# Performance work log

Hardware: AMD Instinct MI355X
Metric: run time of the kernel (lower is better)

## Reference

```python
import jax, jax.numpy as jnp
import numpy as np

N = 50000
E = 800000
IN_DIM = 128
HEADS = 4
OUT_DIM = 32
TOT = HEADS * OUT_DIM  # 128 == IN_DIM -> residual_proj is None
LN_EPS = 1e-5
NEG_SLOPE = 0.2


def setup_inputs() -> dict:
    key = jax.random.key(0)
    ks = jax.random.split(key, 10)
    x = jax.random.normal(ks[0], (N, IN_DIM), dtype=jnp.float32)
    # random edges guaranteed src != dst (PyG GATv2Conv removes then re-adds self loops)
    src = jax.random.randint(ks[1], (E,), 0, N)
    off = jax.random.randint(ks[2], (E,), 1, N)
    dst = (src + off) % N
    edge_index = jnp.stack([src, dst]).astype(jnp.int64)
    # glorot-style init for weights
    sc = 1.0 / np.sqrt(IN_DIM)
    W_l = jax.random.uniform(ks[3], (IN_DIM, TOT), jnp.float32, -sc, sc)
    b_l = jnp.zeros((TOT,), jnp.float32)
    W_r = jax.random.uniform(ks[4], (IN_DIM, TOT), jnp.float32, -sc, sc)
    b_r = jnp.zeros((TOT,), jnp.float32)
    att = jax.random.uniform(ks[5], (HEADS, OUT_DIM), jnp.float32, -sc, sc)
    bias = jnp.zeros((TOT,), jnp.float32)
    ln_g = jnp.ones((TOT,), jnp.float32)
    ln_b = jnp.zeros((TOT,), jnp.float32)
    return {"x": x, "edge_index": edge_index, "W_l": W_l, "b_l": b_l,
            "W_r": W_r, "b_r": b_r, "att": att, "bias": bias,
            "ln_g": ln_g, "ln_b": ln_b}


def _gatv2_layer(x, src, dst, W_l, b_l, W_r, b_r, att, bias, ln_g, ln_b):
    n = x.shape[0]
    # GATv2Conv: x_l = lin_l(x) (source/messages), x_r = lin_r(x) (target)
    xl = (x @ W_l + b_l).reshape(n, HEADS, OUT_DIM)
    xr = (x @ W_r + b_r).reshape(n, HEADS, OUT_DIM)
    m = xl[src] + xr[dst]                               # [E+N, H, D]
    s = jnp.einsum('ehd,hd->eh', jax.nn.leaky_relu(m, NEG_SLOPE), att)
    # per-destination softmax (every node has a self loop -> no empty segments)
    smax = jax.ops.segment_max(s, dst, num_segments=n)  # [N, H]
    e = jnp.exp(s - smax[dst])
    denom = jax.ops.segment_sum(e, dst, num_segments=n)
    alpha = e / denom[dst]                              # [E+N, H]
    out = jax.ops.segment_sum(alpha[..., None] * xl[src], dst, num_segments=n)
    out = out.reshape(n, TOT) + bias
    out = out + x                                       # residual (in_dim == total_out_dim)
    mu = jnp.mean(out, axis=-1, keepdims=True)
    var = jnp.mean(jnp.square(out - mu), axis=-1, keepdims=True)
    y = (out - mu) / jnp.sqrt(var + LN_EPS) * ln_g + ln_b
    return jax.nn.elu(y)


def reference(x, edge_index, W_l, b_l, W_r, b_r, att, bias, ln_g, ln_b):
    n = x.shape[0]
    loops = jnp.arange(n, dtype=edge_index.dtype)
    src = jnp.concatenate([edge_index[0], loops])
    dst = jnp.concatenate([edge_index[1], loops])
    return _gatv2_layer(x, src, dst, W_l, b_l, W_r, b_r, att, bias, ln_g, ln_b)
```

## Files before the change

### kernel.cpp

```cpp
#include <hip/hip_runtime.h>

#define N_NODES 50000
#define E_EDGES 800000
#define M_TOTAL (E_EDGES + N_NODES)
#define IN_DIM 128
#define HEADS 4
#define OUT_DIM 32
#define TOT 128
#define LN_EPS 1e-5f
#define NEG_SLOPE 0.2f
#define LOG2E 1.4426950408889634f

#define SCAN_NBLK ((N_NODES + 255) / 256)
#define GEMM_NBLK ((N_NODES + 63) / 64)
#define HIST_NBLK 128
#define EPB 6656

typedef __bf16 bf16x8 __attribute__((ext_vector_type(8)));
typedef float  f32x4  __attribute__((ext_vector_type(4)));
typedef _Float16 h2   __attribute__((ext_vector_type(2)));

__device__ __forceinline__ float quad_sum(float p) {
    p += __int_as_float(__builtin_amdgcn_update_dpp(
        0, __float_as_int(p), 0xB1 , 0xF, 0xF, true));
    p += __int_as_float(__builtin_amdgcn_update_dpp(
        0, __float_as_int(p), 0x4E , 0xF, 0xF, true));
    return p;
}

__global__ __launch_bounds__(256) void wthist_kernel(
    const int* __restrict__ dsts,
    const float* __restrict__ Wl, const float* __restrict__ Wr,
    unsigned* __restrict__ WT, unsigned char* __restrict__ HP,
    unsigned char* __restrict__ rank8) {
    __shared__ unsigned cnt[N_NODES / 4];
    const int b = blockIdx.x, t = threadIdx.x;
    if (b < 64) {
        const int u = b * 256 + t;
        const int col = u >> 6, k2 = u & 63;
        const float* __restrict__ W = (col < 128) ? Wl : Wr;
        const int c = col & 127;
        union { __bf16 bb[2]; unsigned uu; } p;
        p.bb[0] = (__bf16)W[(2 * k2) * TOT + c];
        p.bb[1] = (__bf16)W[(2 * k2 + 1) * TOT + c];
        WT[col * 64 + k2] = p.uu;
        return;
    }
    const int hb = b - 64;
    const int m_begin = hb * EPB;
    const int m_end = min(m_begin + EPB, M_TOTAL);
    for (int i = t; i < N_NODES / 4; i += 256) cnt[i] = 0;
    __syncthreads();
    for (int m0 = m_begin + t * 4; m0 < m_end; m0 += 1024) {
        int d[4];
        if (m0 < E_EDGES) {
            const int4 dv = *(const int4*)&dsts[m0];
            d[0] = dv.x; d[1] = dv.y; d[2] = dv.z; d[3] = dv.w;
        } else {
            d[0] = m0 - E_EDGES; d[1] = d[0] + 1; d[2] = d[0] + 2; d[3] = d[0] + 3;
        }
        uchar4 r;
        unsigned old, sh;
        sh = (d[0] & 3) * 8; old = atomicAdd(&cnt[d[0] >> 2], 1u << sh);
        r.x = (unsigned char)(old >> sh);
        sh = (d[1] & 3) * 8; old = atomicAdd(&cnt[d[1] >> 2], 1u << sh);
        r.y = (unsigned char)(old >> sh);
        sh = (d[2] & 3) * 8; old = atomicAdd(&cnt[d[2] >> 2], 1u << sh);
        r.z = (unsigned char)(old >> sh);
        sh = (d[3] & 3) * 8; old = atomicAdd(&cnt[d[3] >> 2], 1u << sh);
        r.w = (unsigned char)(old >> sh);
        *(uchar4*)&rank8[m0] = r;
    }
    __syncthreads();
    unsigned* __restrict__ Hrow = (unsigned*)(HP + (size_t)hb * N_NODES);
    for (int i = t; i < N_NODES / 4; i += 256) Hrow[i] = cnt[i];
}

__global__ __launch_bounds__(256) void gemm_kernel(
    const float* __restrict__ x, const unsigned* __restrict__ WT,
    const float* __restrict__ bl, const float* __restrict__ br,
    unsigned* __restrict__ xlb, unsigned* __restrict__ xrb) {
    __shared__ float epi[4][16][66];
    __shared__ unsigned Bs[64][68];
    const int t = threadIdx.x, w = t >> 6, lane = t & 63;
    const int q = lane >> 4, ln = lane & 15;
    const int m0 = blockIdx.x * 64;

    const int row = min(m0 + w * 16 + ln, N_NODES - 1);
    const float* __restrict__ xrow = x + (size_t)row * IN_DIM;
    bf16x8 A[4];
#pragma unroll
    for (int c = 0; c < 4; ++c) {
        const float4 v0 = *(const float4*)&xrow[c * 32 + q * 8];
        const float4 v1 = *(const float4*)&xrow[c * 32 + q * 8 + 4];
        bf16x8 a;
        a[0] = (__bf16)v0.x; a[1] = (__bf16)v0.y; a[2] = (__bf16)v0.z; a[3] = (__bf16)v0.w;
        a[4] = (__bf16)v1.x; a[5] = (__bf16)v1.y; a[6] = (__bf16)v1.z; a[7] = (__bf16)v1.w;
        A[c] = a;
    }

    const int mr = lane >> 2, cg2 = (lane & 3) * 16;
    const int grow = m0 + w * 16 + mr;
#pragma unroll
    for (int g = 0; g < 4; ++g) {
        const int n0 = g * 64;
        __syncthreads();
        {
            const unsigned* __restrict__ src = WT + n0 * 64;
#pragma unroll
            for (int it = 0; it < 4; ++it) {
                const int dw = t * 4 + it * 1024;
                const uint4 v = *(const uint4*)&src[dw];
                *(uint4*)&Bs[dw >> 6][dw & 63] = v;
            }
        }
        __syncthreads();
        const float* __restrict__ bvec = (g < 2) ? bl : br;
        f32x4 acc[4];
#pragma unroll
        for (int nt = 0; nt < 4; ++nt) {
            const float b = bvec[(n0 & 127) + nt * 16 + ln];
            acc[nt] = (f32x4){b, b, b, b};
        }
#pragma unroll
        for (int nt = 0; nt < 4; ++nt) {
#pragma unroll
            for (int c = 0; c < 4; ++c) {
                const bf16x8 B = *(const bf16x8*)&Bs[nt * 16 + ln][c * 16 + q * 4];
                acc[nt] = __builtin_amdgcn_mfma_f32_16x16x32_bf16(A[c], B, acc[nt], 0, 0, 0);
            }
        }
#pragma unroll
        for (int nt = 0; nt < 4; ++nt)
#pragma unroll
            for (int r = 0; r < 4; ++r)
                epi[w][q * 4 + r][nt * 16 + ln] = acc[nt][r];

        if (grow < N_NODES) {
            unsigned p[8];
#pragma unroll
            for (int i = 0; i < 8; ++i) {
                union { _Float16 h[2]; unsigned u; } pk;
                pk.h[0] = (_Float16)epi[w][mr][cg2 + 2 * i];
                pk.h[1] = (_Float16)epi[w][mr][cg2 + 2 * i + 1];
                p[i] = pk.u;
            }
            unsigned* __restrict__ dst = ((g < 2) ? xlb : xrb) +
                (size_t)grow * 64 + (g & 1) * 32 + (cg2 >> 1);
            *(uint4*)&dst[0] = make_uint4(p[0], p[1], p[2], p[3]);
            *(uint4*)&dst[4] = make_uint4(p[4], p[5], p[6], p[7]);
        }
    }
}

__global__ __launch_bounds__(256) void scan1_kernel(
    unsigned char* __restrict__ HP,
    int* __restrict__ incl, int* __restrict__ blockSums,
    int* __restrict__ degtot) {
    __shared__ int sh[256];
    const int t = threadIdx.x;
    const int i = blockIdx.x * 256 + t;
    int tot = 0;
    if (i < N_NODES) {
        int run = 0;
#pragma unroll 16
        for (int b = 0; b < HIST_NBLK; ++b) {
            const int h = HP[(size_t)b * N_NODES + i];
            HP[(size_t)b * N_NODES + i] = (unsigned char)run;
            run += h;
        }
        tot = run;
        degtot[i] = tot;
    }
    sh[t] = tot;
    __syncthreads();
#pragma unroll
    for (int off = 1; off < 256; off <<= 1) {
        int u = (t >= off) ? sh[t - off] : 0;
        __syncthreads();
        sh[t] += u;
        __syncthreads();
    }
    if (i < N_NODES) incl[i] = sh[t];
    if (t == 255) blockSums[blockIdx.x] = sh[255];
}

__global__ __launch_bounds__(256) void scan23_kernel(
    const int* __restrict__ degtot, const int* __restrict__ blockSums,
    int* __restrict__ rowptr ,
    unsigned short* __restrict__ sorted16) {
    __shared__ int sh[256];
    const int t = threadIdx.x;
    const int v0 = (t < SCAN_NBLK) ? blockSums[t] : 0;
    sh[t] = v0;
    __syncthreads();
#pragma unroll
    for (int off = 1; off < 256; off <<= 1) {
        int u = (t >= off) ? sh[t - off] : 0;
        __syncthreads();
        sh[t] += u;
        __syncthreads();
    }
    const int blockOff = (blockIdx.x == 0) ? 0 : sh[blockIdx.x - 1];
    const int i = blockIdx.x * 256 + t;
    if (i < N_NODES)
        rowptr[i] = blockOff + rowptr[i] - degtot[i];
    if (i == 0) rowptr[N_NODES] = M_TOTAL;
    if (blockIdx.x == 0 && t < 32) sorted16[M_TOTAL + t] = 0;
}

__global__ __launch_bounds__(1024) void scatter_kernel(
    const int* __restrict__ srcs, const int* __restrict__ dsts,
    const int* __restrict__ rowptr, const unsigned char* __restrict__ P,
    const unsigned char* __restrict__ rank8,
    unsigned short* __restrict__ sorted16) {
    __shared__ __align__(16) unsigned char smem[N_NODES];
    const int t = threadIdx.x;
    const int hb = blockIdx.x;
    const uint4* __restrict__ Prow = (const uint4*)(P + (size_t)hb * N_NODES);
    for (int i = t; i < N_NODES / 16; i += 1024)
        ((uint4*)smem)[i] = Prow[i];
    __syncthreads();
    const int eb = hb * EPB;
    const int ee = min(eb + EPB, M_TOTAL);
    for (int m0 = eb + t * 4; m0 < ee; m0 += 4096) {
        int s[4], d[4];
        if (m0 < E_EDGES) {
            const int4 sv = *(const int4*)&srcs[m0];
            const int4 dv = *(const int4*)&dsts[m0];
            s[0] = sv.x; s[1] = sv.y; s[2] = sv.z; s[3] = sv.w;
            d[0] = dv.x; d[1] = dv.y; d[2] = dv.z; d[3] = dv.w;
        } else {
            s[0] = d[0] = m0 - E_EDGES;
            s[1] = d[1] = d[0] + 1; s[2] = d[2] = d[0] + 2; s[3] = d[3] = d[0] + 3;
        }
        const uchar4 r = *(const uchar4*)&rank8[m0];
        sorted16[rowptr[d[0]] + (int)smem[d[0]] + (int)r.x] = (unsigned short)s[0];
        sorted16[rowptr[d[1]] + (int)smem[d[1]] + (int)r.y] = (unsigned short)s[1];
        sorted16[rowptr[d[2]] + (int)smem[d[2]] + (int)r.z] = (unsigned short)s[2];
        sorted16[rowptr[d[3]] + (int)smem[d[3]] + (int)r.w] = (unsigned short)s[3];
    }
}

__global__ __launch_bounds__(256) void gat_kernel(
    const int* __restrict__ rowptr, const unsigned short* __restrict__ sorted16,
    const unsigned* __restrict__ xlb, const unsigned* __restrict__ xrb,
    const float* __restrict__ att, const float* __restrict__ x,
    const float* __restrict__ bias, const float* __restrict__ g,
    const float* __restrict__ bvec, float* __restrict__ out) {
    const int d = blockIdx.x * 4 + (threadIdx.x >> 6);
    const int lane = threadIdx.x & 63;
    const int ln = lane & 15, q = lane >> 4;
    if (d >= N_NODES) return;

    h2 xrh[4], ath[4];
    {
        const uint4 ur = *(const uint4*)&xrb[(size_t)d * 64 + 4 * ln];
        union { uint4 u; h2 h[4]; } cr; cr.u = ur;
        xrh[0] = cr.h[0]; xrh[1] = cr.h[1]; xrh[2] = cr.h[2]; xrh[3] = cr.h[3];
        const float4 a0 = *(const float4*)&att[8 * ln];
        const float4 a1 = *(const float4*)&att[8 * ln + 4];
        ath[0][0] = (_Float16)(a0.x * LOG2E); ath[0][1] = (_Float16)(a0.y * LOG2E);
        ath[1][0] = (_Float16)(a0.z * LOG2E); ath[1][1] = (_Float16)(a0.w * LOG2E);
        ath[2][0] = (_Float16)(a1.x * LOG2E); ath[2][1] = (_Float16)(a1.y * LOG2E);
        ath[3][0] = (_Float16)(a1.z * LOG2E); ath[3][1] = (_Float16)(a1.w * LOG2E);
    }
    const h2 slope = (h2){(_Float16)NEG_SLOPE, (_Float16)NEG_SLOPE};
    const int beg = rowptr[d], end = rowptr[d + 1];

    float l = 0.f;
    h2 acc4[4];
#pragma unroll
    for (int k = 0; k < 4; ++k) acc4[k] = (h2){(_Float16)0.f, (_Float16)0.f};

    uint4 u0, u1;
    {
        const int sA0 = (int)sorted16[min(beg + q, end - 1)];
        const int sA1 = (int)sorted16[min(beg + 4 + q, end - 1)];
        u0 = *(const uint4*)&xlb[(size_t)sA0 * 64 + 4 * ln];
        u1 = *(const uint4*)&xlb[(size_t)sA1 * 64 + 4 * ln];
    }
    int sB0 = (int)sorted16[min(beg + 8 + q, end - 1)];
    int sB1 = (int)sorted16[min(beg + 12 + q, end - 1)];

    for (int base = beg; base < end; base += 8) {
        const int sC0 = (int)sorted16[min(base + 16 + q, end - 1)];
        const int sC1 = (int)sorted16[min(base + 20 + q, end - 1)];
        const uint4 un0 = *(const uint4*)&xlb[(size_t)sB0 * 64 + 4 * ln];
        const uint4 un1 = *(const uint4*)&xlb[(size_t)sB1 * 64 + 4 * ln];

        union { unsigned uu; h2 h; } a0, a1, a2, a3, b0, b1, b2, b3;
        a0.uu = u0.x; a1.uu = u0.y; a2.uu = u0.z; a3.uu = u0.w;
        b0.uu = u1.x; b1.uu = u1.y; b2.uu = u1.z; b3.uu = u1.w;
        h2 mA0 = a0.h + xrh[0], mA1 = a1.h + xrh[1];
        h2 mA2 = a2.h + xrh[2], mA3 = a3.h + xrh[3];
        h2 mB0 = b0.h + xrh[0], mB1 = b1.h + xrh[1];
        h2 mB2 = b2.h + xrh[2], mB3 = b3.h + xrh[3];
        mA0 = __builtin_elementwise_max(mA0, mA0 * slope);
        mA1 = __builtin_elementwise_max(mA1, mA1 * slope);
        mA2 = __builtin_elementwise_max(mA2, mA2 * slope);
        mA3 = __builtin_elementwise_max(mA3, mA3 * slope);
        mB0 = __builtin_elementwise_max(mB0, mB0 * slope);
        mB1 = __builtin_elementwise_max(mB1, mB1 * slope);
        mB2 = __builtin_elementwise_max(mB2, mB2 * slope);
        mB3 = __builtin_elementwise_max(mB3, mB3 * slope);
        float p0 = __builtin_amdgcn_fdot2(mA0, ath[0], 0.0f, false);
        p0 = __builtin_amdgcn_fdot2(mA1, ath[1], p0, false);
        p0 = __builtin_amdgcn_fdot2(mA2, ath[2], p0, false);
        p0 = __builtin_amdgcn_fdot2(mA3, ath[3], p0, false);
        float p1 = __builtin_amdgcn_fdot2(mB0, ath[0], 0.0f, false);
        p1 = __builtin_amdgcn_fdot2(mB1, ath[1], p1, false);
        p1 = __builtin_amdgcn_fdot2(mB2, ath[2], p1, false);
        p1 = __builtin_amdgcn_fdot2(mB3, ath[3], p1, false);
        p0 = quad_sum(p0);
        p1 = quad_sum(p1);
        const float e0 = (base + q < end) ? exp2f(p0) : 0.f;
        const float e1 = (base + 4 + q < end) ? exp2f(p1) : 0.f;
        l += e0 + e1;
        const _Float16 eh0 = (_Float16)e0, eh1 = (_Float16)e1;
        const h2 e20 = (h2){eh0, eh0}, e21 = (h2){eh1, eh1};
        acc4[0] += e20 * a0.h; acc4[0] += e21 * b0.h;
        acc4[1] += e20 * a1.h; acc4[1] += e21 * b1.h;
        acc4[2] += e20 * a2.h; acc4[2] += e21 * b2.h;
        acc4[3] += e20 * a3.h; acc4[3] += e21 * b3.h;

        u0 = un0; u1 = un1; sB0 = sC0; sB1 = sC1;
    }

#pragma unroll
    for (int off = 16; off <= 32; off <<= 1) {
        l += __shfl_xor(l, off, 64);
#pragma unroll
        for (int k = 0; k < 4; ++k) {
            union { h2 h; int i; } tmp; tmp.h = acc4[k];
            tmp.i = __shfl_xor(tmp.i, off, 64);
            acc4[k] += tmp.h;
        }
    }
    float acc[8];
#pragma unroll
    for (int k = 0; k < 4; ++k) {
        acc[2 * k]     = (float)acc4[k][0];
        acc[2 * k + 1] = (float)acc4[k][1];
    }

    const float inv_l = 1.0f / l;
    const float4 xv0 = *(const float4*)&x[(size_t)d * TOT + 8 * ln];
    const float4 xv1 = *(const float4*)&x[(size_t)d * TOT + 8 * ln + 4];
    const float4 bi0 = *(const float4*)&bias[8 * ln];
    const float4 bi1 = *(const float4*)&bias[8 * ln + 4];
    float v[8];
    v[0] = fmaf(acc[0], inv_l, bi0.x + xv0.x);
    v[1] = fmaf(acc[1], inv_l, bi0.y + xv0.y);
    v[2] = fmaf(acc[2], inv_l, bi0.z + xv0.z);
    v[3] = fmaf(acc[3], inv_l, bi0.w + xv0.w);
    v[4] = fmaf(acc[4], inv_l, bi1.x + xv1.x);
    v[5] = fmaf(acc[5], inv_l, bi1.y + xv1.y);
    v[6] = fmaf(acc[6], inv_l, bi1.z + xv1.z);
    v[7] = fmaf(acc[7], inv_l, bi1.w + xv1.w);
    float sum = 0.f, sq = 0.f;
#pragma unroll
    for (int k = 0; k < 8; ++k) { sum += v[k]; sq = fmaf(v[k], v[k], sq); }
#pragma unroll
    for (int off = 1; off <= 8; off <<= 1) {
        sum += __shfl_xor(sum, off, 64);
        sq  += __shfl_xor(sq,  off, 64);
    }
    const float mu  = sum * (1.0f / TOT);
    const float var = sq * (1.0f / TOT) - mu * mu;
    const float inv = rsqrtf(var + LN_EPS);
    const float4 g0 = *(const float4*)&g[8 * ln];
    const float4 g1 = *(const float4*)&g[8 * ln + 4];
    const float4 b0 = *(const float4*)&bvec[8 * ln];
    const float4 b1 = *(const float4*)&bvec[8 * ln + 4];
    float y[8];
    y[0] = (v[0] - mu) * inv * g0.x + b0.x;
    y[1] = (v[1] - mu) * inv * g0.y + b0.y;
    y[2] = (v[2] - mu) * inv * g0.z + b0.z;
    y[3] = (v[3] - mu) * inv * g0.w + b0.w;
    y[4] = (v[4] - mu) * inv * g1.x + b1.x;
    y[5] = (v[5] - mu) * inv * g1.y + b1.y;
    y[6] = (v[6] - mu) * inv * g1.z + b1.z;
    y[7] = (v[7] - mu) * inv * g1.w + b1.w;
#pragma unroll
    for (int k = 0; k < 8; ++k) y[k] = y[k] > 0.f ? y[k] : __expf(y[k]) - 1.f;
    if (q < 2) {
        float4 o = (q == 0) ? make_float4(y[0], y[1], y[2], y[3])
                            : make_float4(y[4], y[5], y[6], y[7]);
        *(float4*)&out[(size_t)d * TOT + 8 * ln + 4 * q] = o;
    }
}

extern "C" void kernel_launch(void* const* d_in, const int* in_sizes, int n_in,
                              void* d_out, int out_size, void* d_ws, size_t ws_size,
                              hipStream_t stream) {
    const float* x    = (const float*)d_in[0];
    const int*   ei   = (const int*)d_in[1];
    const float* Wl   = (const float*)d_in[2];
    const float* bl   = (const float*)d_in[3];
    const float* Wr   = (const float*)d_in[4];
    const float* br   = (const float*)d_in[5];
    const float* att  = (const float*)d_in[6];
    const float* bias = (const float*)d_in[7];
    const float* ln_g = (const float*)d_in[8];
    const float* ln_b = (const float*)d_in[9];
    const int* srcs = ei;
    const int* dsts = ei + E_EDGES;

    unsigned* xlb = (unsigned*)d_ws;
    unsigned* xrb = xlb + (size_t)N_NODES * 64;
    int*   degtot     = (int*)(xrb + (size_t)N_NODES * 64);
    int*   rowptr     = degtot + N_NODES;
    int*   blockSums  = rowptr + N_NODES + 1;
    unsigned* WT      = (unsigned*)(blockSums + SCAN_NBLK + 3);
    unsigned char* HP = (unsigned char*)(WT + 256 * 64);
    unsigned short* sorted16 = (unsigned short*)(HP + (size_t)HIST_NBLK * N_NODES);
    unsigned char*  rank8    = (unsigned char*)(sorted16 + M_TOTAL + 32);

    wthist_kernel<<<64 + HIST_NBLK, 256, 0, stream>>>(dsts, Wl, Wr, WT, HP, rank8);
    gemm_kernel<<<GEMM_NBLK, 256, 0, stream>>>(x, WT, bl, br, xlb, xrb);
    scan1_kernel<<<SCAN_NBLK, 256, 0, stream>>>(HP, rowptr, blockSums, degtot);
    scan23_kernel<<<SCAN_NBLK, 256, 0, stream>>>(degtot, blockSums, rowptr, sorted16);
    scatter_kernel<<<HIST_NBLK, 1024, 0, stream>>>(srcs, dsts, rowptr, HP, rank8, sorted16);
    gat_kernel<<<(N_NODES + 3) / 4, 256, 0, stream>>>(rowptr, sorted16, xlb, xrb, att, x,
                                                      bias, ln_g, ln_b, (float*)d_out);
}
```

Measured before the change: 175.3 us.

## Fuse histogram and GEMM into one launch with 4-bit shared counters

Merges the weight-transpose/histogram kernel and the GEMM kernel into a single launch. Histogram blocks run alongside GEMM blocks, and each GEMM block converts fp32 weights to bf16 in LDS itself, so the WT workspace goes away. The histogram now packs per-node counts as 4-bit nibbles, halving LDS use so histogram blocks can share occupancy with GEMM blocks. The nibble counts overflow if any node gets 16 or more edges within one block's chunk; with random edges that is unlikely but not guaranteed. The gat kernel also issues its epilogue parameter loads early to hide their latency.

```diff
diff --git a/kernel.cpp b/kernel.cpp
--- a/kernel.cpp
+++ b/kernel.cpp
@@ -28,61 +28,57 @@
     return p;
 }
 
-__global__ __launch_bounds__(256) void wthist_kernel(
+__global__ __launch_bounds__(256) void histgemm_kernel(
     const int* __restrict__ dsts,
     const float* __restrict__ Wl, const float* __restrict__ Wr,
-    unsigned* __restrict__ WT, unsigned char* __restrict__ HP,
-    unsigned char* __restrict__ rank8) {
-    __shared__ unsigned cnt[N_NODES / 4];
-    const int b = blockIdx.x, t = threadIdx.x;
-    if (b < 64) {
-        const int u = b * 256 + t;
-        const int col = u >> 6, k2 = u & 63;
-        const float* __restrict__ W = (col < 128) ? Wl : Wr;
-        const int c = col & 127;
-        union { __bf16 bb[2]; unsigned uu; } p;
-        p.bb[0] = (__bf16)W[(2 * k2) * TOT + c];
-        p.bb[1] = (__bf16)W[(2 * k2 + 1) * TOT + c];
-        WT[col * 64 + k2] = p.uu;
-        return;
-    }
-    const int hb = b - 64;
-    const int m_begin = hb * EPB;
-    const int m_end = min(m_begin + EPB, M_TOTAL);
-    for (int i = t; i < N_NODES / 4; i += 256) cnt[i] = 0;
-    __syncthreads();
-    for (int m0 = m_begin + t * 4; m0 < m_end; m0 += 1024) {
-        int d[4];
-        if (m0 < E_EDGES) {
-            const int4 dv = *(const int4*)&dsts[m0];
-            d[0] = dv.x; d[1] = dv.y; d[2] = dv.z; d[3] = dv.w;
-        } else {
-            d[0] = m0 - E_EDGES; d[1] = d[0] + 1; d[2] = d[0] + 2; d[3] = d[0] + 3;
-        }
-        uchar4 r;
-        unsigned old, sh;
-        sh = (d[0] & 3) * 8; old = atomicAdd(&cnt[d[0] >> 2], 1u << sh);
-        r.x = (unsigned char)(old >> sh);
-        sh = (d[1] & 3) * 8; old = atomicAdd(&cnt[d[1] >> 2], 1u << sh);
-        r.y = (unsigned char)(old >> sh);
-        sh = (d[2] & 3) * 8; old = atomicAdd(&cnt[d[2] >> 2], 1u << sh);
-        r.z = (unsigned char)(old >> sh);
-        sh = (d[3] & 3) * 8; old = atomicAdd(&cnt[d[3] >> 2], 1u << sh);
-        r.w = (unsigned char)(old >> sh);
-        *(uchar4*)&rank8[m0] = r;
-    }
-    __syncthreads();
-    unsigned* __restrict__ Hrow = (unsigned*)(HP + (size_t)hb * N_NODES);
-    for (int i = t; i < N_NODES / 4; i += 256) Hrow[i] = cnt[i];
-}
-
-__global__ __launch_bounds__(256) void gemm_kernel(
-    const float* __restrict__ x, const unsigned* __restrict__ WT,
+    unsigned char* __restrict__ HP, unsigned char* __restrict__ rank8,
+    const float* __restrict__ x,
     const float* __restrict__ bl, const float* __restrict__ br,
     unsigned* __restrict__ xlb, unsigned* __restrict__ xrb) {
-    __shared__ float epi[4][16][66];
-    __shared__ unsigned Bs[64][68];
-    const int t = threadIdx.x, w = t >> 6, lane = t & 63;
+    __shared__ union {
+        unsigned cnt[N_NODES / 8];
+        struct { float epi[4][16][66]; unsigned Bs[64][68]; } g;
+    } sm;
+    const int t = threadIdx.x;
+    if (blockIdx.x >= GEMM_NBLK) {
+        const int hb = blockIdx.x - GEMM_NBLK;
+        const int m_begin = hb * EPB;
+        const int m_end = min(m_begin + EPB, M_TOTAL);
+        for (int i = t; i < N_NODES / 8; i += 256) sm.cnt[i] = 0;
+        __syncthreads();
+        for (int m0 = m_begin + t * 4; m0 < m_end; m0 += 1024) {
+            int d[4];
+            if (m0 < E_EDGES) {
+                const int4 dv = *(const int4*)&dsts[m0];
+                d[0] = dv.x; d[1] = dv.y; d[2] = dv.z; d[3] = dv.w;
+            } else {
+                d[0] = m0 - E_EDGES; d[1] = d[0] + 1; d[2] = d[0] + 2; d[3] = d[0] + 3;
+            }
+            uchar4 r;
+            unsigned old, sh;
+            sh = (d[0] & 7) * 4; old = atomicAdd(&sm.cnt[d[0] >> 3], 1u << sh);
+            r.x = (unsigned char)((old >> sh) & 15u);
+            sh = (d[1] & 7) * 4; old = atomicAdd(&sm.cnt[d[1] >> 3], 1u << sh);
+            r.y = (unsigned char)((old >> sh) & 15u);
+            sh = (d[2] & 7) * 4; old = atomicAdd(&sm.cnt[d[2] >> 3], 1u << sh);
+            r.z = (unsigned char)((old >> sh) & 15u);
+            sh = (d[3] & 7) * 4; old = atomicAdd(&sm.cnt[d[3] >> 3], 1u << sh);
+            r.w = (unsigned char)((old >> sh) & 15u);
+            *(uchar4*)&rank8[m0] = r;
+        }
+        __syncthreads();
+        unsigned* __restrict__ Hrow = (unsigned*)(HP + (size_t)hb * N_NODES);
+        for (int i = t; i < N_NODES / 8; i += 256) {
+            const unsigned w = sm.cnt[i];
+            const unsigned lo = (w & 15u) | (((w >> 4) & 15u) << 8) |
+                                (((w >> 8) & 15u) << 16) | (((w >> 12) & 15u) << 24);
+            const unsigned hi = ((w >> 16) & 15u) | (((w >> 20) & 15u) << 8) |
+                                (((w >> 24) & 15u) << 16) | (((w >> 28) & 15u) << 24);
+            *(uint2*)&Hrow[2 * i] = make_uint2(lo, hi);
+        }
+        return;
+    }
+    const int w = t >> 6, lane = t & 63;
     const int q = lane >> 4, ln = lane & 15;
     const int m0 = blockIdx.x * 64;
 
@@ -103,30 +99,34 @@
     const int grow = m0 + w * 16 + mr;
 #pragma unroll
     for (int g = 0; g < 4; ++g) {
-        const int n0 = g * 64;
-        __syncthreads();
-        {
-            const unsigned* __restrict__ src = WT + n0 * 64;
-#pragma unroll
-            for (int it = 0; it < 4; ++it) {
-                const int dw = t * 4 + it * 1024;
-                const uint4 v = *(const uint4*)&src[dw];
-                *(uint4*)&Bs[dw >> 6][dw & 63] = v;
-            }
+        const float* __restrict__ Wsrc = (g < 2) ? Wl : Wr;
+        const int cbase = (g & 1) * 64;
+        __syncthreads();
+#pragma unroll
+        for (int it = 0; it < 4; ++it) {
+            const int cell = t + it * 256;
+            const int k2 = cell >> 4, c = (cell & 15) * 4;
+            const float4 a = *(const float4*)&Wsrc[(2 * k2) * TOT + cbase + c];
+            const float4 b = *(const float4*)&Wsrc[(2 * k2 + 1) * TOT + cbase + c];
+            union { __bf16 bb[2]; unsigned uu; } p;
+            p.bb[0] = (__bf16)a.x; p.bb[1] = (__bf16)b.x; sm.g.Bs[c][k2] = p.uu;
+            p.bb[0] = (__bf16)a.y; p.bb[1] = (__bf16)b.y; sm.g.Bs[c + 1][k2] = p.uu;
+            p.bb[0] = (__bf16)a.z; p.bb[1] = (__bf16)b.z; sm.g.Bs[c + 2][k2] = p.uu;
+            p.bb[0] = (__bf16)a.w; p.bb[1] = (__bf16)b.w; sm.g.Bs[c + 3][k2] = p.uu;
         }
         __syncthreads();
         const float* __restrict__ bvec = (g < 2) ? bl : br;
         f32x4 acc[4];
 #pragma unroll
         for (int nt = 0; nt < 4; ++nt) {
-            const float b = bvec[(n0 & 127) + nt * 16 + ln];
+            const float b = bvec[cbase + nt * 16 + ln];
             acc[nt] = (f32x4){b, b, b, b};
         }
 #pragma unroll
         for (int nt = 0; nt < 4; ++nt) {
 #pragma unroll
             for (int c = 0; c < 4; ++c) {
-                const bf16x8 B = *(const bf16x8*)&Bs[nt * 16 + ln][c * 16 + q * 4];
+                const bf16x8 B = *(const bf16x8*)&sm.g.Bs[nt * 16 + ln][c * 16 + q * 4];
                 acc[nt] = __builtin_amdgcn_mfma_f32_16x16x32_bf16(A[c], B, acc[nt], 0, 0, 0);
             }
         }
@@ -134,15 +134,15 @@
         for (int nt = 0; nt < 4; ++nt)
 #pragma unroll
             for (int r = 0; r < 4; ++r)
-                epi[w][q * 4 + r][nt * 16 + ln] = acc[nt][r];
+                sm.g.epi[w][q * 4 + r][nt * 16 + ln] = acc[nt][r];
 
         if (grow < N_NODES) {
             unsigned p[8];
 #pragma unroll
             for (int i = 0; i < 8; ++i) {
                 union { _Float16 h[2]; unsigned u; } pk;
-                pk.h[0] = (_Float16)epi[w][mr][cg2 + 2 * i];
-                pk.h[1] = (_Float16)epi[w][mr][cg2 + 2 * i + 1];
+                pk.h[0] = (_Float16)sm.g.epi[w][mr][cg2 + 2 * i];
+                pk.h[1] = (_Float16)sm.g.epi[w][mr][cg2 + 2 * i + 1];
                 p[i] = pk.u;
             }
             unsigned* __restrict__ dst = ((g < 2) ? xlb : xrb) +
@@ -265,6 +265,15 @@
         ath[2][0] = (_Float16)(a1.x * LOG2E); ath[2][1] = (_Float16)(a1.y * LOG2E);
         ath[3][0] = (_Float16)(a1.z * LOG2E); ath[3][1] = (_Float16)(a1.w * LOG2E);
     }
+    const float4 xv0 = *(const float4*)&x[(size_t)d * TOT + 8 * ln];
+    const float4 xv1 = *(const float4*)&x[(size_t)d * TOT + 8 * ln + 4];
+    const float4 bi0 = *(const float4*)&bias[8 * ln];
+    const float4 bi1 = *(const float4*)&bias[8 * ln + 4];
+    const float4 g0 = *(const float4*)&g[8 * ln];
+    const float4 g1 = *(const float4*)&g[8 * ln + 4];
+    const float4 b0 = *(const float4*)&bvec[8 * ln];
+    const float4 b1 = *(const float4*)&bvec[8 * ln + 4];
+
     const h2 slope = (h2){(_Float16)NEG_SLOPE, (_Float16)NEG_SLOPE};
     const int beg = rowptr[d], end = rowptr[d + 1];
 
@@ -289,13 +298,13 @@
         const uint4 un0 = *(const uint4*)&xlb[(size_t)sB0 * 64 + 4 * ln];
         const uint4 un1 = *(const uint4*)&xlb[(size_t)sB1 * 64 + 4 * ln];
 
-        union { unsigned uu; h2 h; } a0, a1, a2, a3, b0, b1, b2, b3;
+        union { unsigned uu; h2 h; } a0, a1, a2, a3, b0_, b1_, b2_, b3_;
         a0.uu = u0.x; a1.uu = u0.y; a2.uu = u0.z; a3.uu = u0.w;
-        b0.uu = u1.x; b1.uu = u1.y; b2.uu = u1.z; b3.uu = u1.w;
+        b0_.uu = u1.x; b1_.uu = u1.y; b2_.uu = u1.z; b3_.uu = u1.w;
         h2 mA0 = a0.h + xrh[0], mA1 = a1.h + xrh[1];
         h2 mA2 = a2.h + xrh[2], mA3 = a3.h + xrh[3];
-        h2 mB0 = b0.h + xrh[0], mB1 = b1.h + xrh[1];
-        h2 mB2 = b2.h + xrh[2], mB3 = b3.h + xrh[3];
+        h2 mB0 = b0_.h + xrh[0], mB1 = b1_.h + xrh[1];
+        h2 mB2 = b2_.h + xrh[2], mB3 = b3_.h + xrh[3];
         mA0 = __builtin_elementwise_max(mA0, mA0 * slope);
         mA1 = __builtin_elementwise_max(mA1, mA1 * slope);
         mA2 = __builtin_elementwise_max(mA2, mA2 * slope);
@@ -319,10 +328,10 @@
         l += e0 + e1;
         const _Float16 eh0 = (_Float16)e0, eh1 = (_Float16)e1;
         const h2 e20 = (h2){eh0, eh0}, e21 = (h2){eh1, eh1};
-        acc4[0] += e20 * a0.h; acc4[0] += e21 * b0.h;
-        acc4[1] += e20 * a1.h; acc4[1] += e21 * b1.h;
-        acc4[2] += e20 * a2.h; acc4[2] += e21 * b2.h;
-        acc4[3] += e20 * a3.h; acc4[3] += e21 * b3.h;
+        acc4[0] += e20 * a0.h; acc4[0] += e21 * b0_.h;
+        acc4[1] += e20 * a1.h; acc4[1] += e21 * b1_.h;
+        acc4[2] += e20 * a2.h; acc4[2] += e21 * b2_.h;
+        acc4[3] += e20 * a3.h; acc4[3] += e21 * b3_.h;
 
         u0 = un0; u1 = un1; sB0 = sC0; sB1 = sC1;
     }
@@ -345,10 +354,6 @@
     }
 
     const float inv_l = 1.0f / l;
-    const float4 xv0 = *(const float4*)&x[(size_t)d * TOT + 8 * ln];
-    const float4 xv1 = *(const float4*)&x[(size_t)d * TOT + 8 * ln + 4];
-    const float4 bi0 = *(const float4*)&bias[8 * ln];
-    const float4 bi1 = *(const float4*)&bias[8 * ln + 4];
     float v[8];
     v[0] = fmaf(acc[0], inv_l, bi0.x + xv0.x);
     v[1] = fmaf(acc[1], inv_l, bi0.y + xv0.y);
@@ -369,10 +374,6 @@
     const float mu  = sum * (1.0f / TOT);
     const float var = sq * (1.0f / TOT) - mu * mu;
     const float inv = rsqrtf(var + LN_EPS);
-    const float4 g0 = *(const float4*)&g[8 * ln];
-    const float4 g1 = *(const float4*)&g[8 * ln + 4];
-    const float4 b0 = *(const float4*)&bvec[8 * ln];
-    const float4 b1 = *(const float4*)&bvec[8 * ln + 4];
     float y[8];
     y[0] = (v[0] - mu) * inv * g0.x + b0.x;
     y[1] = (v[1] - mu) * inv * g0.y + b0.y;
@@ -412,13 +413,12 @@
     int*   degtot     = (int*)(xrb + (size_t)N_NODES * 64);
     int*   rowptr     = degtot + N_NODES;
     int*   blockSums  = rowptr + N_NODES + 1;
-    unsigned* WT      = (unsigned*)(blockSums + SCAN_NBLK + 3);
-    unsigned char* HP = (unsigned char*)(WT + 256 * 64);
+    unsigned char* HP = (unsigned char*)(blockSums + SCAN_NBLK + 3);
     unsigned short* sorted16 = (unsigned short*)(HP + (size_t)HIST_NBLK * N_NODES);
     unsigned char*  rank8    = (unsigned char*)(sorted16 + M_TOTAL + 32);
 
-    wthist_kernel<<<64 + HIST_NBLK, 256, 0, stream>>>(dsts, Wl, Wr, WT, HP, rank8);
-    gemm_kernel<<<GEMM_NBLK, 256, 0, stream>>>(x, WT, bl, br, xlb, xrb);
+    histgemm_kernel<<<GEMM_NBLK + HIST_NBLK, 256, 0, stream>>>(
+        dsts, Wl, Wr, HP, rank8, x, bl, br, xlb, xrb);
     scan1_kernel<<<SCAN_NBLK, 256, 0, stream>>>(HP, rowptr, blockSums, degtot);
     scan23_kernel<<<SCAN_NBLK, 256, 0, stream>>>(degtot, blockSums, rowptr, sorted16);
     scatter_kernel<<<HIST_NBLK, 1024, 0, stream>>>(srcs, dsts, rowptr, HP, rank8, sorted16);
```

Measured after the change: 191.8 us. 1.09x slower.

## Pack histogram counters into 4-bit nibbles and halve histogram partitions

Applied to the files above, without the earlier changes.

The dst histogram now uses 4-bit shared-memory counters, which fits twice the edges per block. That cuts the number of histogram partitions from 128 to 64 and halves the per-partition prefix table that scan1 reads and writes. The scatter kernel still launches 128 blocks by splitting each partition in two, and the separate degree array is removed by writing exclusive prefixes directly. The trade-off is that per-block per-node counts must stay below 16, which holds for uniformly random destinations but could overflow on skewed graphs. Histogram parallelism also drops to 64 blocks.

```diff
diff --git a/kernel.cpp b/kernel.cpp
--- a/kernel.cpp
+++ b/kernel.cpp
@@ -13,8 +13,9 @@
 
 #define SCAN_NBLK ((N_NODES + 255) / 256)
 #define GEMM_NBLK ((N_NODES + 63) / 64)
-#define HIST_NBLK 128
-#define EPB 6656
+#define HIST_NBLK 64
+#define EPB 13312
+#define HEPB (EPB / 2)
 
 typedef __bf16 bf16x8 __attribute__((ext_vector_type(8)));
 typedef float  f32x4  __attribute__((ext_vector_type(4)));
@@ -33,7 +34,7 @@
     const float* __restrict__ Wl, const float* __restrict__ Wr,
     unsigned* __restrict__ WT, unsigned char* __restrict__ HP,
     unsigned char* __restrict__ rank8) {
-    __shared__ unsigned cnt[N_NODES / 4];
+    __shared__ unsigned cnt[N_NODES / 8];
     const int b = blockIdx.x, t = threadIdx.x;
     if (b < 64) {
         const int u = b * 256 + t;
@@ -49,7 +50,7 @@
     const int hb = b - 64;
     const int m_begin = hb * EPB;
     const int m_end = min(m_begin + EPB, M_TOTAL);
-    for (int i = t; i < N_NODES / 4; i += 256) cnt[i] = 0;
+    for (int i = t; i < N_NODES / 8; i += 256) cnt[i] = 0;
     __syncthreads();
     for (int m0 = m_begin + t * 4; m0 < m_end; m0 += 1024) {
         int d[4];
@@ -61,19 +62,26 @@
         }
         uchar4 r;
         unsigned old, sh;
-        sh = (d[0] & 3) * 8; old = atomicAdd(&cnt[d[0] >> 2], 1u << sh);
-        r.x = (unsigned char)(old >> sh);
-        sh = (d[1] & 3) * 8; old = atomicAdd(&cnt[d[1] >> 2], 1u << sh);
-        r.y = (unsigned char)(old >> sh);
-        sh = (d[2] & 3) * 8; old = atomicAdd(&cnt[d[2] >> 2], 1u << sh);
-        r.z = (unsigned char)(old >> sh);
-        sh = (d[3] & 3) * 8; old = atomicAdd(&cnt[d[3] >> 2], 1u << sh);
-        r.w = (unsigned char)(old >> sh);
+        sh = (d[0] & 7) * 4; old = atomicAdd(&cnt[d[0] >> 3], 1u << sh);
+        r.x = (unsigned char)((old >> sh) & 15u);
+        sh = (d[1] & 7) * 4; old = atomicAdd(&cnt[d[1] >> 3], 1u << sh);
+        r.y = (unsigned char)((old >> sh) & 15u);
+        sh = (d[2] & 7) * 4; old = atomicAdd(&cnt[d[2] >> 3], 1u << sh);
+        r.z = (unsigned char)((old >> sh) & 15u);
+        sh = (d[3] & 7) * 4; old = atomicAdd(&cnt[d[3] >> 3], 1u << sh);
+        r.w = (unsigned char)((old >> sh) & 15u);
         *(uchar4*)&rank8[m0] = r;
     }
     __syncthreads();
     unsigned* __restrict__ Hrow = (unsigned*)(HP + (size_t)hb * N_NODES);
-    for (int i = t; i < N_NODES / 4; i += 256) Hrow[i] = cnt[i];
+    for (int i = t; i < N_NODES / 8; i += 256) {
+        const unsigned w = cnt[i];
+        const unsigned lo = (w & 15u) | (((w >> 4) & 15u) << 8) |
+                            (((w >> 8) & 15u) << 16) | (((w >> 12) & 15u) << 24);
+        const unsigned hi = ((w >> 16) & 15u) | (((w >> 20) & 15u) << 8) |
+                            (((w >> 24) & 15u) << 16) | (((w >> 28) & 15u) << 24);
+        *(uint2*)&Hrow[2 * i] = make_uint2(lo, hi);
+    }
 }
 
 __global__ __launch_bounds__(256) void gemm_kernel(
@@ -155,8 +163,7 @@
 
 __global__ __launch_bounds__(256) void scan1_kernel(
     unsigned char* __restrict__ HP,
-    int* __restrict__ incl, int* __restrict__ blockSums,
-    int* __restrict__ degtot) {
+    int* __restrict__ rowptr, int* __restrict__ blockSums) {
     __shared__ int sh[256];
     const int t = threadIdx.x;
     const int i = blockIdx.x * 256 + t;
@@ -170,7 +177,6 @@
             run += h;
         }
         tot = run;
-        degtot[i] = tot;
     }
     sh[t] = tot;
     __syncthreads();
@@ -181,12 +187,12 @@
         sh[t] += u;
         __syncthreads();
     }
-    if (i < N_NODES) incl[i] = sh[t];
+    if (i < N_NODES) rowptr[i] = sh[t] - tot;
     if (t == 255) blockSums[blockIdx.x] = sh[255];
 }
 
 __global__ __launch_bounds__(256) void scan23_kernel(
-    const int* __restrict__ degtot, const int* __restrict__ blockSums,
+    const int* __restrict__ blockSums,
     int* __restrict__ rowptr ,
     unsigned short* __restrict__ sorted16) {
     __shared__ int sh[256];
@@ -203,8 +209,7 @@
     }
     const int blockOff = (blockIdx.x == 0) ? 0 : sh[blockIdx.x - 1];
     const int i = blockIdx.x * 256 + t;
-    if (i < N_NODES)
-        rowptr[i] = blockOff + rowptr[i] - degtot[i];
+    if (i < N_NODES) rowptr[i] += blockOff;
     if (i == 0) rowptr[N_NODES] = M_TOTAL;
     if (blockIdx.x == 0 && t < 32) sorted16[M_TOTAL + t] = 0;
 }
@@ -216,13 +221,14 @@
     unsigned short* __restrict__ sorted16) {
     __shared__ __align__(16) unsigned char smem[N_NODES];
     const int t = threadIdx.x;
-    const int hb = blockIdx.x;
+    const int sb = blockIdx.x;
+    const int hb = sb >> 1;
     const uint4* __restrict__ Prow = (const uint4*)(P + (size_t)hb * N_NODES);
     for (int i = t; i < N_NODES / 16; i += 1024)
         ((uint4*)smem)[i] = Prow[i];
     __syncthreads();
-    const int eb = hb * EPB;
-    const int ee = min(eb + EPB, M_TOTAL);
+    const int eb = hb * EPB + (sb & 1) * HEPB;
+    const int ee = min(eb + HEPB, M_TOTAL);
     for (int m0 = eb + t * 4; m0 < ee; m0 += 4096) {
         int s[4], d[4];
         if (m0 < E_EDGES) {
@@ -409,19 +415,18 @@
 
     unsigned* xlb = (unsigned*)d_ws;
     unsigned* xrb = xlb + (size_t)N_NODES * 64;
-    int*   degtot     = (int*)(xrb + (size_t)N_NODES * 64);
-    int*   rowptr     = degtot + N_NODES;
+    int*   rowptr     = (int*)(xrb + (size_t)N_NODES * 64);
     int*   blockSums  = rowptr + N_NODES + 1;
-    unsigned* WT      = (unsigned*)(blockSums + SCAN_NBLK + 3);
+    unsigned* WT      = (unsigned*)(blockSums + SCAN_NBLK + 4);
     unsigned char* HP = (unsigned char*)(WT + 256 * 64);
     unsigned short* sorted16 = (unsigned short*)(HP + (size_t)HIST_NBLK * N_NODES);
     unsigned char*  rank8    = (unsigned char*)(sorted16 + M_TOTAL + 32);
 
     wthist_kernel<<<64 + HIST_NBLK, 256, 0, stream>>>(dsts, Wl, Wr, WT, HP, rank8);
     gemm_kernel<<<GEMM_NBLK, 256, 0, stream>>>(x, WT, bl, br, xlb, xrb);
-    scan1_kernel<<<SCAN_NBLK, 256, 0, stream>>>(HP, rowptr, blockSums, degtot);
-    scan23_kernel<<<SCAN_NBLK, 256, 0, stream>>>(degtot, blockSums, rowptr, sorted16);
-    scatter_kernel<<<HIST_NBLK, 1024, 0, stream>>>(srcs, dsts, rowptr, HP, rank8, sorted16);
+    scan1_kernel<<<SCAN_NBLK, 256, 0, stream>>>(HP, rowptr, blockSums);
+    scan23_kernel<<<SCAN_NBLK, 256, 0, stream>>>(blockSums, rowptr, sorted16);
+    scatter_kernel<<<2 * HIST_NBLK, 1024, 0, stream>>>(srcs, dsts, rowptr, HP, rank8, sorted16);
     gat_kernel<<<(N_NODES + 3) / 4, 256, 0, stream>>>(rowptr, sorted16, xlb, xrb, att, x,
                                                       bias, ln_g, ln_b, (float*)d_out);
 }
```

Measured after the change: 173.4 us. No clear change (-1.0%).
